# Kernel tuning notes

Hardware: AMD Instinct MI355X
Metric: run time of the kernel (lower is better)

Reference implementation:

```python
import jax, jax.numpy as jnp
import numpy as np

N = 100_000      # nodes
E = 3_200_000    # edges (avg degree 32)
F_IN = 64        # num_node_features
G = 256          # graphs in batch


def _lin(key, fan_in, fan_out):
    kw, kb = jax.random.split(key)
    bound = 1.0 / np.sqrt(fan_in)
    W = jax.random.uniform(kw, (fan_in, fan_out), jnp.float32, -bound, bound)
    b = jax.random.uniform(kb, (fan_out,), jnp.float32, -bound, bound)
    return W, b


def setup_inputs() -> dict:
    key = jax.random.key(0)
    ks = jax.random.split(key, 9)
    x = jax.random.normal(ks[0], (N, F_IN), jnp.float32)
    edge_index = jax.random.randint(ks[1], (2, E), 0, N, dtype=jnp.int64)
    batch = jnp.sort(jax.random.randint(ks[2], (N,), 0, G, dtype=jnp.int64))
    W1, b1 = _lin(ks[3], F_IN, 60)
    W2, b2 = _lin(ks[4], 60, 50)
    Wf1, bf1 = _lin(ks[5], 50, 30)
    Wf2, bf2 = _lin(ks[6], 30, 20)
    Wf3, bf3 = _lin(ks[7], 20, 10)
    Wo, bo = _lin(ks[8], 10, 1)
    return {"x": x, "edge_index": edge_index, "batch": batch,
            "W1": W1, "b1": b1, "W2": W2, "b2": b2,
            "Wf1": Wf1, "bf1": bf1, "Wf2": Wf2, "bf2": bf2,
            "Wf3": Wf3, "bf3": bf3, "Wo": Wo, "bo": bo}


def _gcn_norm(edge_index, n_nodes):
    # add self loops, then symmetric D^{-1/2} (A+I) D^{-1/2} edge weights
    loop = jnp.arange(n_nodes, dtype=edge_index.dtype)
    src = jnp.concatenate([edge_index[0], loop])
    dst = jnp.concatenate([edge_index[1], loop])
    deg = jax.ops.segment_sum(jnp.ones_like(dst, dtype=jnp.float32), dst,
                              num_segments=n_nodes)
    dinv = jax.lax.rsqrt(deg)  # deg >= 1 thanks to self loops
    norm = dinv[src] * dinv[dst]
    return src, dst, norm


def _gcn_conv(h, W, b, src, dst, norm, n_nodes):
    h = h @ W                                            # [N, out]
    msg = h[src] * norm[:, None]                         # gather over edges
    agg = jax.ops.segment_sum(msg, dst, num_segments=n_nodes)
    return agg + b


def reference(x, edge_index, batch, W1, b1, W2, b2,
              Wf1, bf1, Wf2, bf2, Wf3, bf3, Wo, bo):
    n_nodes = x.shape[0]
    src, dst, norm = _gcn_norm(edge_index, n_nodes)
    h = _gcn_conv(x, W1, b1, src, dst, norm, n_nodes)    # [N, 60]
    h = _gcn_conv(h, W2, b2, src, dst, norm, n_nodes)    # [N, 50]
    # global_add_pool over graph ids
    g = jax.ops.segment_sum(h, batch, num_segments=G)    # [G, 50]
    # MLP stack (no nonlinearities in the original forward)
    g = g @ Wf1 + bf1
    g = g @ Wf2 + bf2
    g = g @ Wf3 + bf3
    return g @ Wo + bo                                   # [G, 1]
```

## Files before the change

### kernel.cpp

```cpp
#include <hip/hip_runtime.h>


#define RSHIFT 7
#define RNODES 128
#define NB_MAX 1024
#define STHREADS 512
#define CTHREADS 512
#define STAGE_CAP 8192
#define BCAP 6144

__global__ void collapse_weights_k(
    const float* __restrict__ W1, const float* __restrict__ b1,
    const float* __restrict__ W2, const float* __restrict__ b2,
    const float* __restrict__ Wf1, const float* __restrict__ bf1,
    const float* __restrict__ Wf2, const float* __restrict__ bf2,
    const float* __restrict__ Wf3, const float* __restrict__ bf3,
    const float* __restrict__ Wo, const float* __restrict__ bo,
    float* __restrict__ w1c, float* __restrict__ sc,
    int* __restrict__ cursor, float* __restrict__ out, int G)
{
    __shared__ float wo[10], w3[20], w2[30], w1[50], w2c[60];
    __shared__ float c0s;
    const int t = threadIdx.x;
    for (int b = t; b < NB_MAX; b += 64) cursor[b] = 0;
    if (t < 10) wo[t] = Wo[t];
    __syncthreads();
    if (t < 20) { float s = 0.f; for (int j = 0; j < 10; ++j) s += Wf3[t*10+j]*wo[j]; w3[t] = s; }
    __syncthreads();
    if (t < 30) { float s = 0.f; for (int j = 0; j < 20; ++j) s += Wf2[t*20+j]*w3[j]; w2[t] = s; }
    __syncthreads();
    if (t < 50) { float s = 0.f; for (int j = 0; j < 30; ++j) s += Wf1[t*30+j]*w2[j]; w1[t] = s; }
    __syncthreads();
    if (t < 60) { float s = 0.f; for (int j = 0; j < 50; ++j) s += W2[t*50+j]*w1[j]; w2c[t] = s; }
    __syncthreads();
    { float s = 0.f; for (int j = 0; j < 60; ++j) s += W1[t*60+j]*w2c[j]; w1c[t] = s; }
    if (t == 0) {
        float c1 = 0.f; for (int j = 0; j < 60; ++j) c1 += b1[j]*w2c[j];
        float c2 = 0.f; for (int j = 0; j < 50; ++j) c2 += b2[j]*w1[j];
        float c0 = bo[0];
        for (int j = 0; j < 30; ++j) c0 += bf1[j]*w2[j];
        for (int j = 0; j < 20; ++j) c0 += bf2[j]*w3[j];
        for (int j = 0; j < 10; ++j) c0 += bf3[j]*wo[j];
        sc[0] = c1; sc[1] = c2; sc[2] = c0;
        c0s = c0;
    }
    __syncthreads();
    for (int g = t; g < G; g += 64) out[g] = c0s;
}

#define LOAD_QUAD(ii, cc, P0, P1, P2, P3, B0, B1, B2, B3, R0, R1, R2, R3)     \
    if (cc == 4) {                                                            \
        int4 s4 = *reinterpret_cast<const int4*>(src + ii);                   \
        int4 d4 = *reinterpret_cast<const int4*>(dst + ii);                   \
        P0 = (unsigned)s4.x | ((unsigned)(d4.x & (RNODES-1)) << 17);          \
        P1 = (unsigned)s4.y | ((unsigned)(d4.y & (RNODES-1)) << 17);          \
        P2 = (unsigned)s4.z | ((unsigned)(d4.z & (RNODES-1)) << 17);          \
        P3 = (unsigned)s4.w | ((unsigned)(d4.w & (RNODES-1)) << 17);          \
        B0 = d4.x >> RSHIFT; B1 = d4.y >> RSHIFT;                             \
        B2 = d4.z >> RSHIFT; B3 = d4.w >> RSHIFT;                             \
        R0 = atomicAdd(&hist[B0], 1);                                         \
        R1 = atomicAdd(&hist[B1], 1);                                         \
        R2 = atomicAdd(&hist[B2], 1);                                         \
        R3 = atomicAdd(&hist[B3], 1);                                         \
    } else {                                                                  \
        if (cc > 0) { int s=src[ii],   d=dst[ii];   P0=(unsigned)s|((unsigned)(d&(RNODES-1))<<17); B0=d>>RSHIFT; R0=atomicAdd(&hist[B0],1); } \
        if (cc > 1) { int s=src[ii+1], d=dst[ii+1]; P1=(unsigned)s|((unsigned)(d&(RNODES-1))<<17); B1=d>>RSHIFT; R1=atomicAdd(&hist[B1],1); } \
        if (cc > 2) { int s=src[ii+2], d=dst[ii+2]; P2=(unsigned)s|((unsigned)(d&(RNODES-1))<<17); B2=d>>RSHIFT; R2=atomicAdd(&hist[B2],1); } \
    }

#define STORE_QUAD(cc, P0, P1, P2, P3, B0, B1, B2, B3, R0, R1, R2, R3)        \
    if (cc > 0) { int s2 = tbase[B0] + R0; staged[s2] = P0; bof[s2] = (unsigned short)B0; } \
    if (cc > 1) { int s2 = tbase[B1] + R1; staged[s2] = P1; bof[s2] = (unsigned short)B1; } \
    if (cc > 2) { int s2 = tbase[B2] + R2; staged[s2] = P2; bof[s2] = (unsigned short)B2; } \
    if (cc > 3) { int s2 = tbase[B3] + R3; staged[s2] = P3; bof[s2] = (unsigned short)B3; }

__global__ __launch_bounds__(STHREADS, 4)
void scatter_u_k(const float* __restrict__ x, const float* __restrict__ w1c,
                 float* __restrict__ u,
                 const int* __restrict__ src, const int* __restrict__ dst,
                 int E, int n, int npb, int nb,
                 int* __restrict__ cursor, unsigned int* __restrict__ binned) {
    __shared__ int hist[NB_MAX];
    __shared__ int tbase[NB_MAX];
    __shared__ int adj[NB_MAX];
    __shared__ int sums[STHREADS];
    __shared__ unsigned int staged[STAGE_CAP];
    __shared__ unsigned short bof[STAGE_CAP];
    const int tid = threadIdx.x;
    const int bx = blockIdx.x;

    {
        const int grp = tid >> 4, sub = tid & 15;
        float4 wv = *reinterpret_cast<const float4*>(w1c + sub * 4);
        int base = bx * npb;
        for (int p = 0; p * 32 < npb; ++p) {
            int nl = p * 32 + grp;
            int g = base + nl;
            bool ok = (nl < npb) && (g < n);
            float val = 0.f;
            if (ok) {
                float4 xv = *reinterpret_cast<const float4*>(
                    x + (size_t)g * 64 + sub * 4);
                val = xv.x*wv.x + xv.y*wv.y + xv.z*wv.z + xv.w*wv.w;
            }
            val += __shfl_down(val, 8, 16);
            val += __shfl_down(val, 4, 16);
            val += __shfl_down(val, 2, 16);
            val += __shfl_down(val, 1, 16);
            if (ok && sub == 0) u[g] = val;
        }
    }

    hist[tid] = 0; hist[tid + STHREADS] = 0;
    __syncthreads();
    int e0 = bx * STAGE_CAP;
    int e1 = e0 + STAGE_CAP; if (e1 > E) e1 = E;

    unsigned pa0=0,pa1=0,pa2=0,pa3=0, pb0=0,pb1=0,pb2=0,pb3=0;
    unsigned pc0=0,pc1=0,pc2=0,pc3=0, pd0=0,pd1=0,pd2=0,pd3=0;
    int ba0=0,ba1=0,ba2=0,ba3=0, bb0=0,bb1=0,bb2=0,bb3=0;
    int bc0=0,bc1=0,bc2=0,bc3=0, bd0=0,bd1=0,bd2=0,bd3=0;
    int ra0=0,ra1=0,ra2=0,ra3=0, rb0=0,rb1=0,rb2=0,rb3=0;
    int rc0=0,rc1=0,rc2=0,rc3=0, rd0=0,rd1=0,rd2=0,rd3=0;

    int iA = e0 + tid * 4;
    int iB = iA + STHREADS * 4;
    int iC = iB + STHREADS * 4;
    int iD = iC + STHREADS * 4;
    int cA = e1 - iA; if (cA > 4) cA = 4; if (cA < 0) cA = 0;
    int cB = e1 - iB; if (cB > 4) cB = 4; if (cB < 0) cB = 0;
    int cC = e1 - iC; if (cC > 4) cC = 4; if (cC < 0) cC = 0;
    int cD = e1 - iD; if (cD > 4) cD = 4; if (cD < 0) cD = 0;

    LOAD_QUAD(iA, cA, pa0,pa1,pa2,pa3, ba0,ba1,ba2,ba3, ra0,ra1,ra2,ra3)
    LOAD_QUAD(iB, cB, pb0,pb1,pb2,pb3, bb0,bb1,bb2,bb3, rb0,rb1,rb2,rb3)
    LOAD_QUAD(iC, cC, pc0,pc1,pc2,pc3, bc0,bc1,bc2,bc3, rc0,rc1,rc2,rc3)
    LOAD_QUAD(iD, cD, pd0,pd1,pd2,pd3, bd0,bd1,bd2,bd3, rd0,rd1,rd2,rd3)
    __syncthreads();

    int h0 = hist[2*tid], h1 = hist[2*tid+1];
    int pair = h0 + h1;
    sums[tid] = pair;
    __syncthreads();
    for (int off = 1; off < STHREADS; off <<= 1) {
        int a = (tid >= off) ? sums[tid - off] : 0;
        __syncthreads();
        sums[tid] += a;
        __syncthreads();
    }
    int excl = sums[tid] - pair;
    tbase[2*tid] = excl;
    tbase[2*tid+1] = excl + h0;
    {
        int b0 = 2*tid, b1 = 2*tid + 1;
        if (b0 < nb && h0 > 0) {
            int r = atomicAdd(&cursor[b0], h0);
            adj[b0] = b0 * BCAP + r - excl;
        }
        if (b1 < nb && h1 > 0) {
            int r = atomicAdd(&cursor[b1], h1);
            adj[b1] = b1 * BCAP + r - (excl + h0);
        }
    }
    __syncthreads();

    STORE_QUAD(cA, pa0,pa1,pa2,pa3, ba0,ba1,ba2,ba3, ra0,ra1,ra2,ra3)
    STORE_QUAD(cB, pb0,pb1,pb2,pb3, bb0,bb1,bb2,bb3, rb0,rb1,rb2,rb3)
    STORE_QUAD(cC, pc0,pc1,pc2,pc3, bc0,bc1,bc2,bc3, rc0,rc1,rc2,rc3)
    STORE_QUAD(cD, pd0,pd1,pd2,pd3, bd0,bd1,bd2,bd3, rd0,rd1,rd2,rd3)
    __syncthreads();

    int tcount = e1 - e0;
    for (int s2 = tid; s2 < tcount; s2 += STHREADS) {
        int b = bof[s2];
        binned[adj[b] + s2] = staged[s2];
    }
}

__global__ __launch_bounds__(CTHREADS, 4)
void sort_dinv_k(unsigned int* __restrict__ binned,
                 const int* __restrict__ cursor,
                 const float* __restrict__ u,
                 float* __restrict__ dinv, float* __restrict__ w,
                 int* __restrict__ offG, int n) {
    __shared__ unsigned eIn[BCAP];
    __shared__ unsigned eOut[BCAP];
    __shared__ int cnt[RNODES];
    __shared__ int off[RNODES];
    __shared__ int pos[RNODES];
    const int tid = threadIdx.x, b = blockIdx.x;
    if (tid < RNODES) cnt[tid] = 0;
    __syncthreads();
    size_t s0 = (size_t)b * BCAP;
    int c = cursor[b];
    if (c > BCAP) c = BCAP;
    int nvec = c >> 2;
    for (int k = tid; k < nvec; k += CTHREADS) {
        uint4 p = *reinterpret_cast<const uint4*>(binned + s0 + 4 * (size_t)k);
        eIn[4*k+0] = p.x; eIn[4*k+1] = p.y; eIn[4*k+2] = p.z; eIn[4*k+3] = p.w;
        atomicAdd(&cnt[p.x >> 17], 1);
        atomicAdd(&cnt[p.y >> 17], 1);
        atomicAdd(&cnt[p.z >> 17], 1);
        atomicAdd(&cnt[p.w >> 17], 1);
    }
    for (int i = 4 * nvec + tid; i < c; i += CTHREADS) {
        unsigned p = binned[s0 + i];
        eIn[i] = p;
        atomicAdd(&cnt[p >> 17], 1);
    }
    __syncthreads();
    int hval = (tid < RNODES) ? cnt[tid] : 0;
    if (tid < RNODES) off[tid] = hval;
    __syncthreads();
    for (int o = 1; o < RNODES; o <<= 1) {
        int a = 0;
        if (tid < RNODES && tid >= o) a = off[tid - o];
        __syncthreads();
        if (tid < RNODES) off[tid] += a;
        __syncthreads();
    }
    if (tid < RNODES) {
        int e = off[tid] - hval;
        off[tid] = e;
        pos[tid] = e;
    }
    __syncthreads();
    for (int i = tid; i < c; i += CTHREADS) {
        unsigned p = eIn[i];
        int r = atomicAdd(&pos[p >> 17], 1);
        eOut[r] = p;
    }
    __syncthreads();
    for (int k = tid; k < nvec; k += CTHREADS) {
        uint4 p;
        p.x = eOut[4*k+0]; p.y = eOut[4*k+1]; p.z = eOut[4*k+2]; p.w = eOut[4*k+3];
        *reinterpret_cast<uint4*>(binned + s0 + 4 * (size_t)k) = p;
    }
    for (int i = 4 * nvec + tid; i < c; i += CTHREADS)
        binned[s0 + i] = eOut[i];
    if (tid < RNODES) {
        int g = (b << RSHIFT) + tid;
        if (g < n) {
            float d = rsqrtf((float)(cnt[tid] + 1));
            dinv[g] = d;
            w[g] = d * u[g];
            offG[g] = off[tid];
        }
    }
}

__global__ __launch_bounds__(CTHREADS, 8)
void conv_mid_k(const unsigned int* __restrict__ binned,
                const int* __restrict__ cursor, const int* __restrict__ offG,
                const float* __restrict__ w, const float* __restrict__ dinv,
                const float* __restrict__ u, const float* __restrict__ sc,
                float* __restrict__ v, float* __restrict__ wb, int n) {
    __shared__ int off_s[RNODES + 1];
    int tid = threadIdx.x, b = blockIdx.x;
    size_t s0 = (size_t)b * BCAP;
    int c = cursor[b];
    if (c > BCAP) c = BCAP;
    if (tid < RNODES) {
        int g = (b << RSHIFT) + tid;
        off_s[tid] = (g < n) ? offG[g] : c;
    }
    if (tid == 0) off_s[RNODES] = c;
    __syncthreads();
    int node = tid >> 2, sub = tid & 3;
    int g = (b << RSHIFT) + node;
    int o0 = off_s[node], o1 = off_s[node + 1];
    float s = 0.f;
    for (int k = o0 + sub; k < o1; k += 4) {
        unsigned p = binned[s0 + k];
        s += w[p & 0x1FFFF];
    }
    s += __shfl_xor(s, 1, 4);
    s += __shfl_xor(s, 2, 4);
    if (sub == 0 && g < n) {
        float di = dinv[g];
        float val = sc[0] + di * s + di * di * u[g];
        v[g] = val;
        wb[g] = di * val;
    }
}

__global__ __launch_bounds__(CTHREADS, 8)
void conv_final_k(const unsigned int* __restrict__ binned,
                  const int* __restrict__ cursor, const int* __restrict__ offG,
                  const float* __restrict__ wbv, const float* __restrict__ dinv,
                  const float* __restrict__ v, const float* __restrict__ sc,
                  const int* __restrict__ batch, float* __restrict__ out, int n) {
    __shared__ int off_s[RNODES + 1];
    __shared__ float tbuf[RNODES];
    __shared__ int gbuf[RNODES];
    int tid = threadIdx.x, b = blockIdx.x;
    size_t s0 = (size_t)b * BCAP;
    int c = cursor[b];
    if (c > BCAP) c = BCAP;
    if (tid < RNODES) {
        int g = (b << RSHIFT) + tid;
        off_s[tid] = (g < n) ? offG[g] : c;
    }
    if (tid == 0) off_s[RNODES] = c;
    __syncthreads();
    int node = tid >> 2, sub = tid & 3;
    int g = (b << RSHIFT) + node;
    int o0 = off_s[node], o1 = off_s[node + 1];
    float s = 0.f;
    for (int k = o0 + sub; k < o1; k += 4) {
        unsigned p = binned[s0 + k];
        s += wbv[p & 0x1FFFF];
    }
    s += __shfl_xor(s, 1, 4);
    s += __shfl_xor(s, 2, 4);
    if (sub == 0) {
        float tval = 0.f; int gid = -1;
        if (g < n) {
            float di = dinv[g];
            tval = sc[1] + di * s + di * di * v[g];
            gid = batch[g];
        }
        tbuf[node] = tval;
        gbuf[node] = gid;
    }
    __syncthreads();
    if (tid < RNODES) {
        int g2 = (b << RSHIFT) + tid;
        if (g2 < n) {
            int gid = gbuf[tid];
            bool head = (tid == 0) || (gbuf[tid - 1] != gid);
            if (head) {
                float sum = 0.f;
                int i2 = tid;
                while (i2 < RNODES && gbuf[i2] == gid) { sum += tbuf[i2]; ++i2; }
                atomicAdd(&out[gid], sum);
            }
        }
    }
}

extern "C" void kernel_launch(void* const* d_in, const int* in_sizes, int n_in,
                              void* d_out, int out_size, void* d_ws, size_t ws_size,
                              hipStream_t stream)
{
    const float* x    = (const float*)d_in[0];
    const int*   ei   = (const int*)d_in[1];
    const int*   batch= (const int*)d_in[2];
    const float* W1   = (const float*)d_in[3];
    const float* b1   = (const float*)d_in[4];
    const float* W2   = (const float*)d_in[5];
    const float* b2   = (const float*)d_in[6];
    const float* Wf1  = (const float*)d_in[7];
    const float* bf1  = (const float*)d_in[8];
    const float* Wf2  = (const float*)d_in[9];
    const float* bf2  = (const float*)d_in[10];
    const float* Wf3  = (const float*)d_in[11];
    const float* bf3  = (const float*)d_in[12];
    const float* Wo   = (const float*)d_in[13];
    const float* bo   = (const float*)d_in[14];
    float* out = (float*)d_out;

    const int n = in_sizes[0] / 64;
    const int E = in_sizes[1] / 2;
    const int G = out_size;
    const int* src = ei;
    const int* dst = ei + E;
    const int nb = (n + RNODES - 1) >> RSHIFT;

    float* ws_f = (float*)d_ws;
    int*   ws_i = (int*)d_ws;
    float* w1c    = ws_f;
    float* sc     = ws_f + 64;
    int*   cursor = ws_i + 128;
    size_t off_u  = 128 + (size_t)NB_MAX;
    float* u      = ws_f + off_u;
    float* dinv   = u + n;
    float* w      = dinv + n;
    float* v      = w + n;
    float* wb     = v + n;
    int*   offG   = ws_i + off_u + 5*(size_t)n;
    size_t off_b  = off_u + 6*(size_t)n;
    off_b = (off_b + 3) & ~(size_t)3;
    unsigned int* binned = (unsigned int*)(ws_f + off_b);

    const int NT = (E + STAGE_CAP - 1) / STAGE_CAP;
    const int npb = (n + NT - 1) / NT;

    hipLaunchKernelGGL(collapse_weights_k, dim3(1), dim3(64), 0, stream,
                       W1, b1, W2, b2, Wf1, bf1, Wf2, bf2, Wf3, bf3, Wo, bo,
                       w1c, sc, cursor, out, G);
    hipLaunchKernelGGL(scatter_u_k, dim3(NT), dim3(STHREADS), 0, stream,
                       x, w1c, u, src, dst, E, n, npb, nb, cursor, binned);
    hipLaunchKernelGGL(sort_dinv_k, dim3(nb), dim3(CTHREADS), 0, stream,
                       binned, cursor, u, dinv, w, offG, n);
    hipLaunchKernelGGL(conv_mid_k, dim3(nb), dim3(CTHREADS), 0, stream,
                       binned, cursor, offG, w, dinv, u, sc, v, wb, n);
    hipLaunchKernelGGL(conv_final_k, dim3(nb), dim3(CTHREADS), 0, stream,
                       binned, cursor, offG, wb, dinv, v, sc, batch, out, n);
}
```

Baseline: 206.5 us.

## Fuse weight collapse into scatter, scatter directly to global, widen conv blocks

Removes the separate single-block weight-collapse kernel: each scatter block recomputes the collapsed weight vector in shared memory, the cursor is zeroed with a memset, and out is initialised in conv_mid. The scatter no longer stages edges in LDS with a block-wide prefix scan; each thread writes straight to its global bin slot using per-bin atomic bases. The conv kernels move to 1024 threads with 8 lanes per node. This saves a launch and the scan and LDS passes, but gives up coalesced bin writes in favour of scattered global stores, and every block redundantly runs the small MLP collapse.

```diff
diff --git a/kernel.cpp b/kernel.cpp
--- a/kernel.cpp
+++ b/kernel.cpp
@@ -5,48 +5,9 @@
 #define RNODES 128
 #define NB_MAX 1024
 #define STHREADS 512
-#define CTHREADS 512
+#define CTHREADS 1024
 #define STAGE_CAP 8192
 #define BCAP 6144
-
-__global__ void collapse_weights_k(
-    const float* __restrict__ W1, const float* __restrict__ b1,
-    const float* __restrict__ W2, const float* __restrict__ b2,
-    const float* __restrict__ Wf1, const float* __restrict__ bf1,
-    const float* __restrict__ Wf2, const float* __restrict__ bf2,
-    const float* __restrict__ Wf3, const float* __restrict__ bf3,
-    const float* __restrict__ Wo, const float* __restrict__ bo,
-    float* __restrict__ w1c, float* __restrict__ sc,
-    int* __restrict__ cursor, float* __restrict__ out, int G)
-{
-    __shared__ float wo[10], w3[20], w2[30], w1[50], w2c[60];
-    __shared__ float c0s;
-    const int t = threadIdx.x;
-    for (int b = t; b < NB_MAX; b += 64) cursor[b] = 0;
-    if (t < 10) wo[t] = Wo[t];
-    __syncthreads();
-    if (t < 20) { float s = 0.f; for (int j = 0; j < 10; ++j) s += Wf3[t*10+j]*wo[j]; w3[t] = s; }
-    __syncthreads();
-    if (t < 30) { float s = 0.f; for (int j = 0; j < 20; ++j) s += Wf2[t*20+j]*w3[j]; w2[t] = s; }
-    __syncthreads();
-    if (t < 50) { float s = 0.f; for (int j = 0; j < 30; ++j) s += Wf1[t*30+j]*w2[j]; w1[t] = s; }
-    __syncthreads();
-    if (t < 60) { float s = 0.f; for (int j = 0; j < 50; ++j) s += W2[t*50+j]*w1[j]; w2c[t] = s; }
-    __syncthreads();
-    { float s = 0.f; for (int j = 0; j < 60; ++j) s += W1[t*60+j]*w2c[j]; w1c[t] = s; }
-    if (t == 0) {
-        float c1 = 0.f; for (int j = 0; j < 60; ++j) c1 += b1[j]*w2c[j];
-        float c2 = 0.f; for (int j = 0; j < 50; ++j) c2 += b2[j]*w1[j];
-        float c0 = bo[0];
-        for (int j = 0; j < 30; ++j) c0 += bf1[j]*w2[j];
-        for (int j = 0; j < 20; ++j) c0 += bf2[j]*w3[j];
-        for (int j = 0; j < 10; ++j) c0 += bf3[j]*wo[j];
-        sc[0] = c1; sc[1] = c2; sc[2] = c0;
-        c0s = c0;
-    }
-    __syncthreads();
-    for (int g = t; g < G; g += 64) out[g] = c0s;
-}
 
 #define LOAD_QUAD(ii, cc, P0, P1, P2, P3, B0, B1, B2, B3, R0, R1, R2, R3)     \
     if (cc == 4) {                                                            \
@@ -68,30 +29,64 @@
         if (cc > 2) { int s=src[ii+2], d=dst[ii+2]; P2=(unsigned)s|((unsigned)(d&(RNODES-1))<<17); B2=d>>RSHIFT; R2=atomicAdd(&hist[B2],1); } \
     }
 
-#define STORE_QUAD(cc, P0, P1, P2, P3, B0, B1, B2, B3, R0, R1, R2, R3)        \
-    if (cc > 0) { int s2 = tbase[B0] + R0; staged[s2] = P0; bof[s2] = (unsigned short)B0; } \
-    if (cc > 1) { int s2 = tbase[B1] + R1; staged[s2] = P1; bof[s2] = (unsigned short)B1; } \
-    if (cc > 2) { int s2 = tbase[B2] + R2; staged[s2] = P2; bof[s2] = (unsigned short)B2; } \
-    if (cc > 3) { int s2 = tbase[B3] + R3; staged[s2] = P3; bof[s2] = (unsigned short)B3; }
+#define STOREG_QUAD(cc, P0, P1, P2, P3, B0, B1, B2, B3, R0, R1, R2, R3)       \
+    if (cc > 0) binned[(size_t)B0 * BCAP + lbase[B0] + R0] = P0;              \
+    if (cc > 1) binned[(size_t)B1 * BCAP + lbase[B1] + R1] = P1;              \
+    if (cc > 2) binned[(size_t)B2 * BCAP + lbase[B2] + R2] = P2;              \
+    if (cc > 3) binned[(size_t)B3 * BCAP + lbase[B3] + R3] = P3;
 
 __global__ __launch_bounds__(STHREADS, 4)
-void scatter_u_k(const float* __restrict__ x, const float* __restrict__ w1c,
-                 float* __restrict__ u,
-                 const int* __restrict__ src, const int* __restrict__ dst,
-                 int E, int n, int npb, int nb,
-                 int* __restrict__ cursor, unsigned int* __restrict__ binned) {
+void scatter_k(const float* __restrict__ x,
+               const int* __restrict__ src, const int* __restrict__ dst,
+               const float* __restrict__ W1, const float* __restrict__ b1,
+               const float* __restrict__ W2, const float* __restrict__ b2,
+               const float* __restrict__ Wf1, const float* __restrict__ bf1,
+               const float* __restrict__ Wf2, const float* __restrict__ bf2,
+               const float* __restrict__ Wf3, const float* __restrict__ bf3,
+               const float* __restrict__ Wo, const float* __restrict__ bo,
+               float* __restrict__ u, float* __restrict__ scG,
+               int E, int n, int npb, int nb,
+               int* __restrict__ cursor, unsigned int* __restrict__ binned) {
     __shared__ int hist[NB_MAX];
-    __shared__ int tbase[NB_MAX];
-    __shared__ int adj[NB_MAX];
-    __shared__ int sums[STHREADS];
-    __shared__ unsigned int staged[STAGE_CAP];
-    __shared__ unsigned short bof[STAGE_CAP];
+    __shared__ int lbase[NB_MAX];
+    __shared__ float wtmp[224];
+    __shared__ float w1c_s[64];
     const int tid = threadIdx.x;
     const int bx = blockIdx.x;
 
     {
+        float* wo  = wtmp;
+        float* w3  = wtmp + 16;
+        float* w2  = wtmp + 48;
+        float* w1  = wtmp + 80;
+        float* w2c = wtmp + 144;
+        hist[tid] = 0; hist[tid + STHREADS] = 0;
+        if (tid < 10) wo[tid] = Wo[tid];
+        __syncthreads();
+        if (tid < 20) { float s = 0.f; for (int j = 0; j < 10; ++j) s += Wf3[tid*10+j]*wo[j]; w3[tid] = s; }
+        __syncthreads();
+        if (tid < 30) { float s = 0.f; for (int j = 0; j < 20; ++j) s += Wf2[tid*20+j]*w3[j]; w2[tid] = s; }
+        __syncthreads();
+        if (tid < 50) { float s = 0.f; for (int j = 0; j < 30; ++j) s += Wf1[tid*30+j]*w2[j]; w1[tid] = s; }
+        __syncthreads();
+        if (tid < 60) { float s = 0.f; for (int j = 0; j < 50; ++j) s += W2[tid*50+j]*w1[j]; w2c[tid] = s; }
+        __syncthreads();
+        if (tid < 64) { float s = 0.f; for (int j = 0; j < 60; ++j) s += W1[tid*60+j]*w2c[j]; w1c_s[tid] = s; }
+        if (bx == 0 && tid == 0) {
+            float c1 = 0.f; for (int j = 0; j < 60; ++j) c1 += b1[j]*w2c[j];
+            float c2 = 0.f; for (int j = 0; j < 50; ++j) c2 += b2[j]*w1[j];
+            float c0 = bo[0];
+            for (int j = 0; j < 30; ++j) c0 += bf1[j]*w2[j];
+            for (int j = 0; j < 20; ++j) c0 += bf2[j]*w3[j];
+            for (int j = 0; j < 10; ++j) c0 += bf3[j]*wo[j];
+            scG[0] = c1; scG[1] = c2; scG[2] = c0;
+        }
+        __syncthreads();
+    }
+
+    {
         const int grp = tid >> 4, sub = tid & 15;
-        float4 wv = *reinterpret_cast<const float4*>(w1c + sub * 4);
+        float4 wv = *reinterpret_cast<const float4*>(&w1c_s[sub * 4]);
         int base = bx * npb;
         for (int p = 0; p * 32 < npb; ++p) {
             int nl = p * 32 + grp;
@@ -111,8 +106,6 @@
         }
     }
 
-    hist[tid] = 0; hist[tid + STHREADS] = 0;
-    __syncthreads();
     int e0 = bx * STAGE_CAP;
     int e1 = e0 + STAGE_CAP; if (e1 > E) e1 = E;
 
@@ -138,46 +131,21 @@
     LOAD_QUAD(iD, cD, pd0,pd1,pd2,pd3, bd0,bd1,bd2,bd3, rd0,rd1,rd2,rd3)
     __syncthreads();
 
-    int h0 = hist[2*tid], h1 = hist[2*tid+1];
-    int pair = h0 + h1;
-    sums[tid] = pair;
-    __syncthreads();
-    for (int off = 1; off < STHREADS; off <<= 1) {
-        int a = (tid >= off) ? sums[tid - off] : 0;
-        __syncthreads();
-        sums[tid] += a;
-        __syncthreads();
-    }
-    int excl = sums[tid] - pair;
-    tbase[2*tid] = excl;
-    tbase[2*tid+1] = excl + h0;
     {
-        int b0 = 2*tid, b1 = 2*tid + 1;
-        if (b0 < nb && h0 > 0) {
-            int r = atomicAdd(&cursor[b0], h0);
-            adj[b0] = b0 * BCAP + r - excl;
-        }
-        if (b1 < nb && h1 > 0) {
-            int r = atomicAdd(&cursor[b1], h1);
-            adj[b1] = b1 * BCAP + r - (excl + h0);
-        }
-    }
-    __syncthreads();
-
-    STORE_QUAD(cA, pa0,pa1,pa2,pa3, ba0,ba1,ba2,ba3, ra0,ra1,ra2,ra3)
-    STORE_QUAD(cB, pb0,pb1,pb2,pb3, bb0,bb1,bb2,bb3, rb0,rb1,rb2,rb3)
-    STORE_QUAD(cC, pc0,pc1,pc2,pc3, bc0,bc1,bc2,bc3, rc0,rc1,rc2,rc3)
-    STORE_QUAD(cD, pd0,pd1,pd2,pd3, bd0,bd1,bd2,bd3, rd0,rd1,rd2,rd3)
-    __syncthreads();
-
-    int tcount = e1 - e0;
-    for (int s2 = tid; s2 < tcount; s2 += STHREADS) {
-        int b = bof[s2];
-        binned[adj[b] + s2] = staged[s2];
-    }
-}
-
-__global__ __launch_bounds__(CTHREADS, 4)
+        int b0 = tid, b1 = tid + STHREADS;
+        int h0 = hist[b0], h1 = hist[b1];
+        if (h0 > 0) lbase[b0] = atomicAdd(&cursor[b0], h0);
+        if (h1 > 0) lbase[b1] = atomicAdd(&cursor[b1], h1);
+    }
+    __syncthreads();
+
+    STOREG_QUAD(cA, pa0,pa1,pa2,pa3, ba0,ba1,ba2,ba3, ra0,ra1,ra2,ra3)
+    STOREG_QUAD(cB, pb0,pb1,pb2,pb3, bb0,bb1,bb2,bb3, rb0,rb1,rb2,rb3)
+    STOREG_QUAD(cC, pc0,pc1,pc2,pc3, bc0,bc1,bc2,bc3, rc0,rc1,rc2,rc3)
+    STOREG_QUAD(cD, pd0,pd1,pd2,pd3, bd0,bd1,bd2,bd3, rd0,rd1,rd2,rd3)
+}
+
+__global__ __launch_bounds__(CTHREADS, 2)
 void sort_dinv_k(unsigned int* __restrict__ binned,
                  const int* __restrict__ cursor,
                  const float* __restrict__ u,
@@ -249,14 +217,16 @@
     }
 }
 
-__global__ __launch_bounds__(CTHREADS, 8)
+__global__ __launch_bounds__(CTHREADS, 2)
 void conv_mid_k(const unsigned int* __restrict__ binned,
                 const int* __restrict__ cursor, const int* __restrict__ offG,
                 const float* __restrict__ w, const float* __restrict__ dinv,
                 const float* __restrict__ u, const float* __restrict__ sc,
-                float* __restrict__ v, float* __restrict__ wb, int n) {
+                float* __restrict__ v, float* __restrict__ wb,
+                float* __restrict__ out, int n, int G) {
     __shared__ int off_s[RNODES + 1];
     int tid = threadIdx.x, b = blockIdx.x;
+    if (b == 0 && tid < G) out[tid] = sc[2];
     size_t s0 = (size_t)b * BCAP;
     int c = cursor[b];
     if (c > BCAP) c = BCAP;
@@ -266,16 +236,17 @@
     }
     if (tid == 0) off_s[RNODES] = c;
     __syncthreads();
-    int node = tid >> 2, sub = tid & 3;
+    int node = tid >> 3, sub = tid & 7;
     int g = (b << RSHIFT) + node;
     int o0 = off_s[node], o1 = off_s[node + 1];
     float s = 0.f;
-    for (int k = o0 + sub; k < o1; k += 4) {
+    for (int k = o0 + sub; k < o1; k += 8) {
         unsigned p = binned[s0 + k];
         s += w[p & 0x1FFFF];
     }
-    s += __shfl_xor(s, 1, 4);
-    s += __shfl_xor(s, 2, 4);
+    s += __shfl_xor(s, 1, 8);
+    s += __shfl_xor(s, 2, 8);
+    s += __shfl_xor(s, 4, 8);
     if (sub == 0 && g < n) {
         float di = dinv[g];
         float val = sc[0] + di * s + di * di * u[g];
@@ -284,7 +255,7 @@
     }
 }
 
-__global__ __launch_bounds__(CTHREADS, 8)
+__global__ __launch_bounds__(CTHREADS, 2)
 void conv_final_k(const unsigned int* __restrict__ binned,
                   const int* __restrict__ cursor, const int* __restrict__ offG,
                   const float* __restrict__ wbv, const float* __restrict__ dinv,
@@ -303,16 +274,17 @@
     }
     if (tid == 0) off_s[RNODES] = c;
     __syncthreads();
-    int node = tid >> 2, sub = tid & 3;
+    int node = tid >> 3, sub = tid & 7;
     int g = (b << RSHIFT) + node;
     int o0 = off_s[node], o1 = off_s[node + 1];
     float s = 0.f;
-    for (int k = o0 + sub; k < o1; k += 4) {
+    for (int k = o0 + sub; k < o1; k += 8) {
         unsigned p = binned[s0 + k];
         s += wbv[p & 0x1FFFF];
     }
-    s += __shfl_xor(s, 1, 4);
-    s += __shfl_xor(s, 2, 4);
+    s += __shfl_xor(s, 1, 8);
+    s += __shfl_xor(s, 2, 8);
+    s += __shfl_xor(s, 4, 8);
     if (sub == 0) {
         float tval = 0.f; int gid = -1;
         if (g < n) {
@@ -369,10 +341,9 @@
 
     float* ws_f = (float*)d_ws;
     int*   ws_i = (int*)d_ws;
-    float* w1c    = ws_f;
-    float* sc     = ws_f + 64;
-    int*   cursor = ws_i + 128;
-    size_t off_u  = 128 + (size_t)NB_MAX;
+    int*   cursor = ws_i;
+    float* scG    = ws_f + NB_MAX;
+    size_t off_u  = NB_MAX + 16;
     float* u      = ws_f + off_u;
     float* dinv   = u + n;
     float* w      = dinv + n;
@@ -386,15 +357,15 @@
     const int NT = (E + STAGE_CAP - 1) / STAGE_CAP;
     const int npb = (n + NT - 1) / NT;
 
-    hipLaunchKernelGGL(collapse_weights_k, dim3(1), dim3(64), 0, stream,
+    hipMemsetAsync(cursor, 0, NB_MAX * sizeof(int), stream);
+    hipLaunchKernelGGL(scatter_k, dim3(NT), dim3(STHREADS), 0, stream,
+                       x, src, dst,
                        W1, b1, W2, b2, Wf1, bf1, Wf2, bf2, Wf3, bf3, Wo, bo,
-                       w1c, sc, cursor, out, G);
-    hipLaunchKernelGGL(scatter_u_k, dim3(NT), dim3(STHREADS), 0, stream,
-                       x, w1c, u, src, dst, E, n, npb, nb, cursor, binned);
+                       u, scG, E, n, npb, nb, cursor, binned);
     hipLaunchKernelGGL(sort_dinv_k, dim3(nb), dim3(CTHREADS), 0, stream,
                        binned, cursor, u, dinv, w, offG, n);
     hipLaunchKernelGGL(conv_mid_k, dim3(nb), dim3(CTHREADS), 0, stream,
-                       binned, cursor, offG, w, dinv, u, sc, v, wb, n);
+                       binned, cursor, offG, w, dinv, u, scG, v, wb, out, n, G);
     hipLaunchKernelGGL(conv_final_k, dim3(nb), dim3(CTHREADS), 0, stream,
-                       binned, cursor, offG, wb, dinv, v, sc, batch, out, n);
-}
+                       binned, cursor, offG, wb, dinv, v, scG, batch, out, n);
+}
```

Result: no change. 204.7 us (-0.9%).
